# Kernel optimization log

Hardware: AMD Instinct MI355X
Metric: run time of the kernel (lower is better)

Reference implementation:

```python
import jax, jax.numpy as jnp
import numpy as np

D_MODEL = 768
D_LAT = 384
N_FREQ = D_MODEL // 2 + 1  # 385
INIT_S = 0.02


def _quat_linear(x, Ww, Wx, Wy, Wz, b):
    # Ww..Wz: [out_q, in_q]; x: [..., 4*in_q]
    d = Ww.shape[1]
    xw, xx, xy, xz = x[..., :d], x[..., d:2*d], x[..., 2*d:3*d], x[..., 3*d:]
    lin = lambda W, v: jnp.einsum('...i,oi->...o', v, W)
    ow = lin(Ww, xw) - lin(Wx, xx) - lin(Wy, xy) - lin(Wz, xz)
    ox = lin(Ww, xx) + lin(Wx, xw) + lin(Wy, xz) - lin(Wz, xy)
    oy = lin(Ww, xy) - lin(Wx, xz) + lin(Wy, xw) + lin(Wz, xx)
    oz = lin(Ww, xz) + lin(Wx, xy) - lin(Wy, xx) + lin(Wz, xw)
    return jnp.concatenate([ow, ox, oy, oz], axis=-1) + b


def _filter1d(x, kr, ki, n):
    X = jnp.fft.rfft(x, axis=-1)
    K = kr + 1j * ki
    return jnp.fft.irfft(X * K, n=n, axis=-1)


def setup_inputs() -> dict:
    key = jax.random.key(0)
    ks = jax.random.split(key, 16)
    rn = lambda k, shape: jax.random.normal(k, shape, dtype=jnp.float32)
    in_q_e, out_q_e = D_MODEL // 4, D_LAT // 4   # 192, 96
    in_q_d, out_q_d = D_LAT // 4, D_MODEL // 4   # 96, 192
    return {
        'x': rn(ks[0], (8, 4096, D_MODEL)),
        'enc_kr': rn(ks[1], (N_FREQ,)) * INIT_S,
        'enc_ki': rn(ks[2], (N_FREQ,)) * INIT_S,
        'dec_kr': rn(ks[3], (N_FREQ,)) * INIT_S,
        'dec_ki': rn(ks[4], (N_FREQ,)) * INIT_S,
        'enc_Ww': rn(ks[5], (out_q_e, in_q_e)) * 0.02,
        'enc_Wx': rn(ks[6], (out_q_e, in_q_e)) * 0.02,
        'enc_Wy': rn(ks[7], (out_q_e, in_q_e)) * 0.02,
        'enc_Wz': rn(ks[8], (out_q_e, in_q_e)) * 0.02,
        'enc_b': jnp.zeros((D_LAT,), jnp.float32),
        'dec_Ww': rn(ks[9], (out_q_d, in_q_d)) * 0.02,
        'dec_Wx': rn(ks[10], (out_q_d, in_q_d)) * 0.02,
        'dec_Wy': rn(ks[11], (out_q_d, in_q_d)) * 0.02,
        'dec_Wz': rn(ks[12], (out_q_d, in_q_d)) * 0.02,
        'dec_b': jnp.zeros((D_MODEL,), jnp.float32),
    }


def reference(x, enc_kr, enc_ki, dec_kr, dec_ki,
              enc_Ww, enc_Wx, enc_Wy, enc_Wz, enc_b,
              dec_Ww, dec_Wx, dec_Wy, dec_Wz, dec_b):
    # encode: spectral filter -> GELU (exact erf, matching nn.GELU) -> quaternion proj
    h = jax.nn.gelu(_filter1d(x, enc_kr, enc_ki, D_MODEL), approximate=False)
    z = _quat_linear(h, enc_Ww, enc_Wx, enc_Wy, enc_Wz, enc_b)
    # decode: quaternion proj -> spectral filter
    recon = _filter1d(_quat_linear(z, dec_Ww, dec_Wx, dec_Wy, dec_Wz, dec_b),
                      dec_kr, dec_ki, D_MODEL)
    loss = jnp.mean((recon - jax.lax.stop_gradient(x)) ** 2)
    return z, loss
```

## Files before the change

kernel.cpp:

```cpp
#include <hip/hip_runtime.h>
#include <hip/hip_bf16.h>
#include <math.h>

typedef unsigned short u16;
typedef __attribute__((ext_vector_type(8))) short s8v;
typedef __attribute__((ext_vector_type(4))) float f4v;

#define DM 768
#define DL 384

__device__ __forceinline__ u16 f2bf(float f) {
  union { float f; unsigned u; } v; v.f = f;
  unsigned r = v.u + 0x7fffu + ((v.u >> 16) & 1u);
  return (u16)(r >> 16);
}
__device__ __forceinline__ float bf2f(u16 b) {
  union { unsigned u; float f; } v; v.u = ((unsigned)b) << 16; return v.f;
}

__global__ void k_build_c2(const float* __restrict__ kr0, const float* __restrict__ ki0,
                           const float* __restrict__ kr1, const float* __restrict__ ki1,
                           float* __restrict__ c0, float* __restrict__ c1) {
  const float* kr = blockIdx.y ? kr1 : kr0;
  const float* ki = blockIdx.y ? ki1 : ki0;
  float* c = blockIdx.y ? c1 : c0;
  const int t = blockIdx.x;
  const int f = threadIdx.x;
  float s = 0.f;
  for (int ff = f; ff < 384; ff += 256) {
    if (ff >= 1) {
      int ph = (ff * t) % DM;
      float th = (float)ph * (6.283185307179586f / DM);
      float sn, cs; sincosf(th, &sn, &cs);
      s += 2.f * (kr[ff] * cs - ki[ff] * sn);
    }
  }
  if (f == 0) s += kr[0] + ((t & 1) ? -kr[384] : kr[384]);
  __shared__ float red[256];
  red[f] = s; __syncthreads();
  for (int k = 128; k > 0; k >>= 1) {
    if (f < k) red[f] += red[f + k];
    __syncthreads();
  }
  if (f == 0) c[t] = red[0] * (1.f / DM);
}

__global__ void k_rb2(const float* __restrict__ c, const float* __restrict__ b,
                      float* __restrict__ rb) {
  const int i = blockIdx.x;
  const int f = threadIdx.x;
  float s = 0.f;
  for (int j = f; j < DM; j += 256) {
    int ci = i - j; if (ci < 0) ci += DM;
    s += c[ci] * b[j];
  }
  __shared__ float red[256];
  red[f] = s; __syncthreads();
  for (int k = 128; k > 0; k >>= 1) {
    if (f < k) red[f] += red[f + k];
    __syncthreads();
  }
  if (f == 0) rb[i] = red[0];
}

__global__ void k_circ2(const float* __restrict__ c0, u16* __restrict__ B0,
                        const float* __restrict__ c1, u16* __restrict__ B1) {
  const float* c = blockIdx.y ? c1 : c0;
  u16* B = blockIdx.y ? B1 : B0;
  int idx = blockIdx.x * 256 + threadIdx.x;
  int i = idx / DM, j = idx % DM;
  int d = i - j; if (d < 0) d += DM;
  B[idx] = f2bf(c[d]);
}

__device__ __constant__ int   MI_[4][4] = {{0,1,2,3},{1,0,3,2},{2,3,0,1},{3,2,1,0}};
__device__ __constant__ float SG_[4][4] = {{1,-1,-1,-1},{1,1,-1,1},{1,1,1,-1},{1,-1,1,1}};

__global__ void k_wenc(const float* __restrict__ Ww, const float* __restrict__ Wx,
                       const float* __restrict__ Wy, const float* __restrict__ Wz,
                       u16* __restrict__ B) {
  int idx = blockIdx.x * 256 + threadIdx.x;
  int o = idx / DM, j = idx % DM;
  int p = o / 96, r = o % 96, q = j / 192, cc = j % 192;
  const float* Ws[4] = {Ww, Wx, Wy, Wz};
  B[idx] = f2bf(SG_[p][q] * Ws[MI_[p][q]][r * 192 + cc]);
}

__global__ void k_ddecT(const float* __restrict__ Ww, const float* __restrict__ Wx,
                        const float* __restrict__ Wy, const float* __restrict__ Wz,
                        u16* __restrict__ B) {
  int idx = blockIdx.x * 256 + threadIdx.x;
  int o = idx / DM, j = idx % DM;
  int p = j / 192, r = j % 192, q = o / 96, cc = o % 96;
  const float* Ws[4] = {Ww, Wx, Wy, Wz};
  B[idx] = f2bf(SG_[p][q] * Ws[MI_[p][q]][r * 96 + cc]);
}

__global__ void k_cvt(const float4* __restrict__ x, u16* __restrict__ xb) {
  int i = blockIdx.x * 256 + threadIdx.x;
  float4 v = x[i];
  union { u16 u[4]; unsigned long long q; } o;
  o.u[0] = f2bf(v.x); o.u[1] = f2bf(v.y); o.u[2] = f2bf(v.z); o.u[3] = f2bf(v.w);
  *(unsigned long long*)(xb + (size_t)i * 4) = o.q;
}

__device__ __forceinline__ void ld_lds16(const u16* g, u16* l) {
  __builtin_amdgcn_global_load_lds((const __attribute__((address_space(1))) void*)g,
                                   (__attribute__((address_space(3))) void*)l, 16, 0, 0);
}

__global__ __launch_bounds__(512, 1) void gemm8_g1(
    const u16* __restrict__ A, const u16* __restrict__ B, u16* __restrict__ outb) {
  __shared__ __align__(16) u16 SM[57344];
  const int t = threadIdx.x;
  const int lane = t & 63, wid = t >> 6;
  const int wrow = wid >> 2, wcol = wid & 3;
  int wg = blockIdx.x;
  { const int q = gridDim.x >> 3; wg = (wg & 7) * q + (wg >> 3); }
  const int bm = wg >> 2, bn = wg & 3;
  constexpr int KT = 768, NT = 768, NKT = KT / 64;

  f4v acc[8][3];
#pragma unroll
  for (int m = 0; m < 8; ++m)
#pragma unroll
    for (int n = 0; n < 3; ++n) acc[m][n] = (f4v)0.f;

  const int srow = t >> 3;
  const int sgrp = (t & 7) ^ (srow & 7);
  const u16* gA = A + (size_t)(bm * 256 + srow) * KT + sgrp * 8;
  const u16* gB = B + (size_t)(bn * 192 + srow) * KT + sgrp * 8;
  const int sx = ((lane >> 4) ^ (lane & 7)) * 8;
  const int ar = (wrow * 128 + (lane & 15)) * 64;
  const int br = 32768 + (wcol * 48 + (lane & 15)) * 64;

  auto stgA = [&](int kt_, int half_) {
    const u16* g = gA + (size_t)(half_ * 128) * KT + kt_ * 64;
    u16* l = SM + (kt_ & 1) * 16384 + half_ * 8192 + t * 8;
    ld_lds16(g, l);
    ld_lds16(g + 64 * KT, l + 4096);
  };
  auto stgB = [&](int kt_, int c_) {
    const u16* g = gB + (size_t)(c_ * 64) * KT + kt_ * 64;
    ld_lds16(g, SM + 32768 + (kt_ & 1) * 12288 + c_ * 4096 + t * 8);
  };

  stgA(0, 0); stgA(0, 1); stgB(0, 0); stgB(0, 1); stgB(0, 2);
  stgA(1, 0); stgB(1, 0);
  asm volatile("s_waitcnt vmcnt(3)" ::: "memory");
  __builtin_amdgcn_sched_barrier(0);
  __builtin_amdgcn_s_barrier();

#pragma unroll 2
  for (int kt = 0; kt < NKT; ++kt) {
    const int ca = (kt & 1) * 16384;
    const int cbb = (kt & 1) * 12288;
    s8v a0[4][2], a1[4][2], b01[2][2], b2[2];
#pragma unroll
    for (int m = 0; m < 4; ++m) {
      a0[m][0] = *(const s8v*)(SM + ca + ar + m * 1024 + sx);
      a0[m][1] = *(const s8v*)(SM + ca + ar + m * 1024 + (sx ^ 32));
    }
#pragma unroll
    for (int n = 0; n < 2; ++n) {
      b01[n][0] = *(const s8v*)(SM + cbb + br + n * 1024 + sx);
      b01[n][1] = *(const s8v*)(SM + cbb + br + n * 1024 + (sx ^ 32));
    }
    if (kt + 1 < NKT) stgA(kt + 1, 1);
    __builtin_amdgcn_s_barrier();
    asm volatile("s_waitcnt lgkmcnt(0)" ::: "memory");
    __builtin_amdgcn_sched_barrier(0);
    __builtin_amdgcn_s_setprio(1);
#pragma unroll
    for (int m = 0; m < 4; ++m)
#pragma unroll
      for (int n = 0; n < 2; ++n) {
        acc[m][n] = __builtin_amdgcn_mfma_f32_16x16x32_bf16(a0[m][0], b01[n][0], acc[m][n], 0, 0, 0);
        acc[m][n] = __builtin_amdgcn_mfma_f32_16x16x32_bf16(a0[m][1], b01[n][1], acc[m][n], 0, 0, 0);
      }
    __builtin_amdgcn_s_setprio(0);
    __builtin_amdgcn_s_barrier();
#pragma unroll
    for (int m = 0; m < 4; ++m) {
      a1[m][0] = *(const s8v*)(SM + ca + ar + (4 + m) * 1024 + sx);
      a1[m][1] = *(const s8v*)(SM + ca + ar + (4 + m) * 1024 + (sx ^ 32));
    }
    if (kt + 1 < NKT) { stgB(kt + 1, 1); stgB(kt + 1, 2); }
    __builtin_amdgcn_s_barrier();
    asm volatile("s_waitcnt lgkmcnt(0)" ::: "memory");
    __builtin_amdgcn_sched_barrier(0);
    __builtin_amdgcn_s_setprio(1);
#pragma unroll
    for (int m = 0; m < 4; ++m)
#pragma unroll
      for (int n = 0; n < 2; ++n) {
        acc[4 + m][n] = __builtin_amdgcn_mfma_f32_16x16x32_bf16(a1[m][0], b01[n][0], acc[4 + m][n], 0, 0, 0);
        acc[4 + m][n] = __builtin_amdgcn_mfma_f32_16x16x32_bf16(a1[m][1], b01[n][1], acc[4 + m][n], 0, 0, 0);
      }
    __builtin_amdgcn_s_setprio(0);
    __builtin_amdgcn_s_barrier();
    b2[0] = *(const s8v*)(SM + cbb + br + 2048 + sx);
    b2[1] = *(const s8v*)(SM + cbb + br + 2048 + (sx ^ 32));
    if (kt + 2 < NKT) stgA(kt + 2, 0);
    __builtin_amdgcn_s_barrier();
    asm volatile("s_waitcnt lgkmcnt(0)" ::: "memory");
    __builtin_amdgcn_sched_barrier(0);
    __builtin_amdgcn_s_setprio(1);
#pragma unroll
    for (int m = 0; m < 4; ++m) {
      acc[4 + m][2] = __builtin_amdgcn_mfma_f32_16x16x32_bf16(a1[m][0], b2[0], acc[4 + m][2], 0, 0, 0);
      acc[4 + m][2] = __builtin_amdgcn_mfma_f32_16x16x32_bf16(a1[m][1], b2[1], acc[4 + m][2], 0, 0, 0);
    }
    __builtin_amdgcn_s_setprio(0);
    __builtin_amdgcn_s_barrier();
    if (kt + 2 < NKT) {
      stgB(kt + 2, 0);
      asm volatile("s_waitcnt vmcnt(3)" ::: "memory");
    } else {
      asm volatile("s_waitcnt vmcnt(0)" ::: "memory");
    }
    __builtin_amdgcn_sched_barrier(0);
    __builtin_amdgcn_s_barrier();
    __builtin_amdgcn_s_setprio(1);
#pragma unroll
    for (int m = 0; m < 4; ++m) {
      acc[m][2] = __builtin_amdgcn_mfma_f32_16x16x32_bf16(a0[m][0], b2[0], acc[m][2], 0, 0, 0);
      acc[m][2] = __builtin_amdgcn_mfma_f32_16x16x32_bf16(a0[m][1], b2[1], acc[m][2], 0, 0, 0);
    }
    __builtin_amdgcn_s_setprio(0);
    __builtin_amdgcn_s_barrier();
  }

  for (int ch = 0; ch < 2; ++ch) {
    if (wrow == ch) {
#pragma unroll
      for (int m = 0; m < 8; ++m)
#pragma unroll
        for (int n = 0; n < 3; ++n)
#pragma unroll
          for (int j = 0; j < 4; ++j) {
            float v = acc[m][n][j];
            float u = v * 0.70710678118f, u2 = u * u;
            float p = u * (1.1283791671f + u2 * (-0.37612638903f +
                      u2 * (0.11283791671f + u2 * (-0.02686617064f))));
            v = 0.5f * v * (1.f + p);
            SM[(m * 16 + (lane >> 4) * 4 + j) * 200 + wcol * 48 + n * 16 + (lane & 15)] = f2bf(v);
          }
    }
    __syncthreads();
#pragma unroll
    for (int it = 0; it < 6; ++it) {
      int idx = it * 512 + t;
      int r = idx / 24, c8 = (idx % 24) * 8;
      s8v vv = *(const s8v*)(SM + r * 200 + c8);
      *(s8v*)(outb + (size_t)(bm * 256 + ch * 128 + r) * NT + bn * 192 + c8) = vv;
    }
    __syncthreads();
  }
}

template <int KT, int NT, int NBN, int EPI, int SWZ>
__global__ __launch_bounds__(256, 3) void gemm_ring(
    const u16* __restrict__ A, const u16* __restrict__ B,
    u16* __restrict__ outb, float* __restrict__ outf,
    const float* __restrict__ bias, const u16* __restrict__ xref,
    float* __restrict__ partials) {
  __shared__ __align__(16) u16 SMR[24576];
#define As_(b) (SMR + (b) * 4096)
#define Bs_(b) (SMR + 12288 + (b) * 4096)
  const int t = threadIdx.x;
  const int wid = t >> 6, lane = t & 63;
  const int wr = wid >> 1, wc = wid & 1;
  int wg = blockIdx.x;
  if (SWZ) { const int q = gridDim.x >> 3; wg = (wg & 7) * q + (wg >> 3); }
  const int bm = wg / NBN, bn = wg % NBN;

  f4v acc[4][4];
#pragma unroll
  for (int m = 0; m < 4; ++m)
#pragma unroll
    for (int n = 0; n < 4; ++n) acc[m][n] = (f4v)0.f;

  const int sgo = ((t & 3) ^ ((t >> 3) & 3)) * 8;
  const u16* gA = A + (size_t)(bm * 128 + (t >> 2)) * KT + sgo;
  const u16* gB = B + (size_t)(bn * 128 + (t >> 2)) * KT + sgo;
  const int fr = lane & 15;
  const int fo = ((lane >> 4) ^ ((fr >> 1) & 3)) * 8;
  constexpr int NK = KT / 32;

  auto stage = [&](int kt_, int b_) {
    const int ko = kt_ * 32;
    ld_lds16(gA + ko, As_(b_) + wid * 512);
    ld_lds16(gA + ko + 64 * KT, As_(b_) + wid * 512 + 2048);
    ld_lds16(gB + ko, Bs_(b_) + wid * 512);
    ld_lds16(gB + ko + 64 * KT, Bs_(b_) + wid * 512 + 2048);
  };

  stage(0, 0);
  stage(1, 1);
#pragma unroll 3
  for (int kt = 0; kt < NK; ++kt) {
    const int b0 = kt % 3, b2 = (kt + 2) % 3;
    if (kt + 2 < NK) stage(kt + 2, b2);
    const int ahead = NK - 1 - kt;
    if (ahead >= 2)      { asm volatile("s_waitcnt vmcnt(8)" ::: "memory"); }
    else if (ahead == 1) { asm volatile("s_waitcnt vmcnt(4)" ::: "memory"); }
    else                 { asm volatile("s_waitcnt vmcnt(0)" ::: "memory"); }
    __builtin_amdgcn_sched_barrier(0);
    __builtin_amdgcn_s_barrier();
    s8v af[4], bfv[4];
#pragma unroll
    for (int m = 0; m < 4; ++m)
      af[m] = *(const s8v*)(As_(b0) + (wr * 64 + m * 16 + fr) * 32 + fo);
#pragma unroll
    for (int n = 0; n < 4; ++n)
      bfv[n] = *(const s8v*)(Bs_(b0) + (wc * 64 + n * 16 + fr) * 32 + fo);
    asm volatile("s_waitcnt lgkmcnt(0)" ::: "memory");
    __builtin_amdgcn_sched_barrier(0);
    __builtin_amdgcn_s_barrier();
    __builtin_amdgcn_s_setprio(1);
#pragma unroll
    for (int m = 0; m < 4; ++m)
#pragma unroll
      for (int n = 0; n < 4; ++n)
        acc[m][n] = __builtin_amdgcn_mfma_f32_16x16x32_bf16(af[m], bfv[n], acc[m][n], 0, 0, 0);
    __builtin_amdgcn_s_setprio(0);
  }

  const int r0l = wr * 64 + ((lane >> 4) << 2);
  const int c0l = wc * 64 + (lane & 15);

  if constexpr (EPI == 2) {
    float bc[4];
#pragma unroll
    for (int n = 0; n < 4; ++n) bc[n] = bias[bn * 128 + c0l + n * 16];
    float ls = 0.f;
#pragma unroll
    for (int m = 0; m < 4; ++m)
#pragma unroll
      for (int n = 0; n < 4; ++n)
#pragma unroll
        for (int j = 0; j < 4; ++j) {
          size_t row = bm * 128 + r0l + m * 16 + j;
          int col = bn * 128 + c0l + n * 16;
          float v = acc[m][n][j] + bc[n];
          float d = v - bf2f(xref[row * NT + col]);
          ls += d * d;
        }
#pragma unroll
    for (int o = 32; o > 0; o >>= 1) ls += __shfl_down(ls, o);
    float* rw = (float*)SMR;
    if (lane == 0) rw[wid] = ls;
    __syncthreads();
    if (t == 0) partials[blockIdx.x] = rw[0] + rw[1] + rw[2] + rw[3];
  } else {
    u16* Cs = SMR;
    float bc[4];
    if constexpr (EPI == 1) {
#pragma unroll
      for (int n = 0; n < 4; ++n) bc[n] = bias[bn * 128 + c0l + n * 16];
    }
#pragma unroll
    for (int m = 0; m < 4; ++m)
#pragma unroll
      for (int n = 0; n < 4; ++n)
#pragma unroll
        for (int j = 0; j < 4; ++j) {
          float v = acc[m][n][j];
          if constexpr (EPI == 1) {
            v += bc[n];
            outf[(size_t)(bm * 128 + r0l + m * 16 + j) * NT + bn * 128 + c0l + n * 16] = v;
          }
          Cs[(r0l + m * 16 + j) * 130 + c0l + n * 16] = f2bf(v);
        }
    __syncthreads();
#pragma unroll
    for (int s = 0; s < 8; ++s) {
      int idx = (s * 256 + t) * 8;
      int r = idx >> 7, c = idx & 127;
      s8v vv = *(const s8v*)(Cs + r * 130 + c);
      *(s8v*)(outb + (size_t)(bm * 128 + r) * NT + bn * 128 + c) = vv;
    }
  }
#undef As_
#undef Bs_
}

__global__ void k_loss_final(const float* __restrict__ partials, float* __restrict__ out) {
  __shared__ float red[256];
  float s = 0.f;
  for (int i = threadIdx.x; i < 1536; i += 256) s += partials[i];
  red[threadIdx.x] = s; __syncthreads();
  for (int k = 128; k > 0; k >>= 1) {
    if (threadIdx.x < k) red[threadIdx.x] += red[threadIdx.x + k];
    __syncthreads();
  }
  if (threadIdx.x == 0) out[0] = red[0] / 25165824.f;
}

extern "C" void kernel_launch(void* const* d_in, const int* in_sizes, int n_in,
                              void* d_out, int out_size, void* d_ws, size_t ws_size,
                              hipStream_t stream) {
  const float* x      = (const float*)d_in[0];
  const float* enc_kr = (const float*)d_in[1];
  const float* enc_ki = (const float*)d_in[2];
  const float* dec_kr = (const float*)d_in[3];
  const float* dec_ki = (const float*)d_in[4];
  const float* enc_Ww = (const float*)d_in[5];
  const float* enc_Wx = (const float*)d_in[6];
  const float* enc_Wy = (const float*)d_in[7];
  const float* enc_Wz = (const float*)d_in[8];
  const float* enc_b  = (const float*)d_in[9];
  const float* dec_Ww = (const float*)d_in[10];
  const float* dec_Wx = (const float*)d_in[11];
  const float* dec_Wy = (const float*)d_in[12];
  const float* dec_Wz = (const float*)d_in[13];
  const float* dec_b  = (const float*)d_in[14];

  char* ws = (char*)d_ws;
  float* c_enc    = (float*)(ws + 0);
  float* c_dec    = (float*)(ws + 4096);
  float* rb       = (float*)(ws + 8192);
  float* partials = (float*)(ws + 12288);
  u16*   Benc     = (u16*)(ws + 20480);
  u16*   Wenc     = (u16*)(ws + 1200128);
  u16*   Mdec     = (u16*)(ws + 1789952);
  u16*   Cdec     = (u16*)(ws + 2379776);
  u16*   DdT      = (u16*)(ws + 3559424);
  u16*   Xb       = (u16*)(ws + 4149248);
  u16*   H        = (u16*)(ws + 54480896);
  u16*   Zb       = (u16*)(ws + 104812544);

  k_build_c2<<<dim3(768, 2), 256, 0, stream>>>(enc_kr, enc_ki, dec_kr, dec_ki, c_enc, c_dec);
  k_rb2<<<768, 256, 0, stream>>>(c_dec, dec_b, rb);
  k_circ2<<<dim3(2304, 2), 256, 0, stream>>>(c_enc, Benc, c_dec, Cdec);
  k_wenc<<<1152, 256, 0, stream>>>(enc_Ww, enc_Wx, enc_Wy, enc_Wz, Wenc);
  k_ddecT<<<1152, 256, 0, stream>>>(dec_Ww, dec_Wx, dec_Wy, dec_Wz, DdT);
  gemm_ring<768, 384, 3, 3, 0><<<18, 256, 0, stream>>>(Cdec, DdT, Mdec, nullptr, nullptr, nullptr, nullptr);
  k_cvt<<<24576, 256, 0, stream>>>((const float4*)x, Xb);

  float* zout = (float*)d_out;
  gemm8_g1<<<512, 512, 0, stream>>>(Xb, Benc, H);
  gemm_ring<768, 384, 3, 1, 1><<<768, 256, 0, stream>>>(H, Wenc, Zb, zout, enc_b, nullptr, nullptr);
  gemm_ring<384, 768, 6, 2, 1><<<1536, 256, 0, stream>>>(Zb, Mdec, nullptr, nullptr, rb, Xb, partials);
  k_loss_final<<<1, 256, 0, stream>>>(partials, zout + (out_size - 1));
}
```

Baseline: 167.1 us.

## Fuse encoder projection and decoder loss GEMMs into one kernel keeping Z in LDS

Replaces the two separate gemm_ring launches (H·Wenc producing Zb in global memory, then Zb·Mdec with loss epilogue) with one kernel. Each block computes a 128x384 Z tile, writes the fp32 z output, and stores a bf16 copy in swizzled LDS. It then runs the decoder GEMM from LDS in two 384-column chunks and accumulates the squared-error loss. This removes the Zb global round-trip and one launch. In exchange the grid drops to 256 blocks at one block per CU, and Mdec fragments are read straight from global memory with no LDS staging or prefetch, which may expose load latency.

```diff
diff --git a/kernel.cpp b/kernel.cpp
--- a/kernel.cpp
+++ b/kernel.cpp
@@ -259,21 +259,154 @@
   }
 }
 
-template <int KT, int NT, int NBN, int EPI, int SWZ>
+__global__ __launch_bounds__(512, 1) void gemm_zl(
+    const u16* __restrict__ H, const u16* __restrict__ Wenc,
+    const u16* __restrict__ Mdec, const u16* __restrict__ Xb,
+    const float* __restrict__ bias, const float* __restrict__ rb,
+    float* __restrict__ zout, float* __restrict__ partials) {
+  __shared__ __align__(16) u16 SM[49152];
+  const int t = threadIdx.x;
+  const int lane = t & 63, wid = t >> 6;
+  const int wrow = wid >> 2, wcol = wid & 3;
+  int wg = blockIdx.x;
+  { const int q = gridDim.x >> 3; wg = (wg & 7) * q + (wg >> 3); }
+  const int bm = wg;
+
+  f4v acc[4][6];
+#pragma unroll
+  for (int m = 0; m < 4; ++m)
+#pragma unroll
+    for (int n = 0; n < 6; ++n) acc[m][n] = (f4v)0.f;
+
+  const int sgo = ((t & 3) ^ ((t >> 3) & 3)) * 8;
+  const u16* gH = H + (size_t)(bm * 128 + (t >> 2)) * 768 + sgo;
+  const u16* gW = Wenc + (size_t)(t >> 2) * 768 + sgo;
+  const int fr = lane & 15;
+  const int fx = ((lane >> 4) ^ ((fr >> 1) & 3)) * 8;
+  const int arow = wrow * 64 + fr;
+
+  auto stage = [&](int kt_, int b_) {
+    ld_lds16(gH + kt_ * 32, SM + b_ * 4096 + t * 8);
+#pragma unroll
+    for (int i = 0; i < 3; ++i)
+      ld_lds16(gW + (size_t)i * 98304 + kt_ * 32, SM + 12288 + b_ * 12288 + i * 4096 + t * 8);
+  };
+
+  stage(0, 0);
+  stage(1, 1);
+#pragma unroll 3
+  for (int kt = 0; kt < 24; ++kt) {
+    const int b0 = kt % 3, b2 = (kt + 2) % 3;
+    if (kt + 2 < 24) stage(kt + 2, b2);
+    const int ahead = 23 - kt;
+    if (ahead >= 2)      { asm volatile("s_waitcnt vmcnt(8)" ::: "memory"); }
+    else if (ahead == 1) { asm volatile("s_waitcnt vmcnt(4)" ::: "memory"); }
+    else                 { asm volatile("s_waitcnt vmcnt(0)" ::: "memory"); }
+    __builtin_amdgcn_sched_barrier(0);
+    __builtin_amdgcn_s_barrier();
+    s8v af[4], bfv[6];
+#pragma unroll
+    for (int m = 0; m < 4; ++m)
+      af[m] = *(const s8v*)(SM + b0 * 4096 + (arow + m * 16) * 32 + fx);
+#pragma unroll
+    for (int n = 0; n < 6; ++n)
+      bfv[n] = *(const s8v*)(SM + 12288 + b0 * 12288 + (wcol * 96 + n * 16 + fr) * 32 + fx);
+    asm volatile("s_waitcnt lgkmcnt(0)" ::: "memory");
+    __builtin_amdgcn_sched_barrier(0);
+    __builtin_amdgcn_s_barrier();
+    __builtin_amdgcn_s_setprio(1);
+#pragma unroll
+    for (int m = 0; m < 4; ++m)
+#pragma unroll
+      for (int n = 0; n < 6; ++n)
+        acc[m][n] = __builtin_amdgcn_mfma_f32_16x16x32_bf16(af[m], bfv[n], acc[m][n], 0, 0, 0);
+    __builtin_amdgcn_s_setprio(0);
+  }
+  __syncthreads();
+
+  float bc[6];
+#pragma unroll
+  for (int n = 0; n < 6; ++n) bc[n] = bias[wcol * 96 + n * 16 + fr];
+#pragma unroll
+  for (int m = 0; m < 4; ++m)
+#pragma unroll
+    for (int n = 0; n < 6; ++n)
+#pragma unroll
+      for (int j = 0; j < 4; ++j) {
+        int rloc = wrow * 64 + m * 16 + (lane >> 4) * 4 + j;
+        int cloc = wcol * 96 + n * 16 + fr;
+        float v = acc[m][n][j] + bc[n];
+        zout[(size_t)(bm * 128 + rloc) * 384 + cloc] = v;
+        int g = cloc >> 3;
+        SM[rloc * 384 + ((g ^ (rloc & 7)) << 3) + (cloc & 7)] = f2bf(v);
+      }
+  __syncthreads();
+
+  float ls = 0.f;
+#pragma unroll 1
+  for (int chunk = 0; chunk < 2; ++chunk) {
+#pragma unroll
+    for (int m = 0; m < 4; ++m)
+#pragma unroll
+      for (int n = 0; n < 6; ++n) acc[m][n] = (f4v)0.f;
+#pragma unroll 3
+    for (int ks = 0; ks < 12; ++ks) {
+      s8v a2[4], b2[6];
+#pragma unroll
+      for (int m = 0; m < 4; ++m) {
+        int r = arow + m * 16;
+        a2[m] = *(const s8v*)(SM + r * 384 + (((ks * 4 + (lane >> 4)) ^ (fr & 7)) << 3));
+      }
+#pragma unroll
+      for (int n = 0; n < 6; ++n) {
+        int cR = chunk * 384 + wcol * 96 + n * 16 + fr;
+        b2[n] = *(const s8v*)(Mdec + (size_t)cR * 384 + ks * 32 + (lane >> 4) * 8);
+      }
+#pragma unroll
+      for (int m = 0; m < 4; ++m)
+#pragma unroll
+        for (int n = 0; n < 6; ++n)
+          acc[m][n] = __builtin_amdgcn_mfma_f32_16x16x32_bf16(a2[m], b2[n], acc[m][n], 0, 0, 0);
+    }
+#pragma unroll
+    for (int m = 0; m < 4; ++m)
+#pragma unroll
+      for (int n = 0; n < 6; ++n) {
+        int cg = chunk * 384 + wcol * 96 + n * 16 + fr;
+        float rbn = rb[cg];
+#pragma unroll
+        for (int j = 0; j < 4; ++j) {
+          int rg = bm * 128 + wrow * 64 + m * 16 + (lane >> 4) * 4 + j;
+          float rec = acc[m][n][j] + rbn;
+          float d = rec - bf2f(Xb[(size_t)rg * 768 + cg]);
+          ls += d * d;
+        }
+      }
+  }
+#pragma unroll
+  for (int o = 32; o > 0; o >>= 1) ls += __shfl_down(ls, o);
+  __syncthreads();
+  float* rw = (float*)SM;
+  if (lane == 0) rw[wid] = ls;
+  __syncthreads();
+  if (t == 0) {
+    float s = 0.f;
+#pragma unroll
+    for (int i = 0; i < 8; ++i) s += rw[i];
+    partials[blockIdx.x] = s;
+  }
+}
+
+template <int KT, int NT, int NBN>
 __global__ __launch_bounds__(256, 3) void gemm_ring(
-    const u16* __restrict__ A, const u16* __restrict__ B,
-    u16* __restrict__ outb, float* __restrict__ outf,
-    const float* __restrict__ bias, const u16* __restrict__ xref,
-    float* __restrict__ partials) {
+    const u16* __restrict__ A, const u16* __restrict__ B, u16* __restrict__ outb) {
   __shared__ __align__(16) u16 SMR[24576];
 #define As_(b) (SMR + (b) * 4096)
 #define Bs_(b) (SMR + 12288 + (b) * 4096)
   const int t = threadIdx.x;
   const int wid = t >> 6, lane = t & 63;
   const int wr = wid >> 1, wc = wid & 1;
-  int wg = blockIdx.x;
-  if (SWZ) { const int q = gridDim.x >> 3; wg = (wg & 7) * q + (wg >> 3); }
-  const int bm = wg / NBN, bn = wg % NBN;
+  const int bm = blockIdx.x / NBN, bn = blockIdx.x % NBN;
 
   f4v acc[4][4];
 #pragma unroll
@@ -329,58 +462,21 @@
 
   const int r0l = wr * 64 + ((lane >> 4) << 2);
   const int c0l = wc * 64 + (lane & 15);
-
-  if constexpr (EPI == 2) {
-    float bc[4];
-#pragma unroll
-    for (int n = 0; n < 4; ++n) bc[n] = bias[bn * 128 + c0l + n * 16];
-    float ls = 0.f;
-#pragma unroll
-    for (int m = 0; m < 4; ++m)
-#pragma unroll
-      for (int n = 0; n < 4; ++n)
-#pragma unroll
-        for (int j = 0; j < 4; ++j) {
-          size_t row = bm * 128 + r0l + m * 16 + j;
-          int col = bn * 128 + c0l + n * 16;
-          float v = acc[m][n][j] + bc[n];
-          float d = v - bf2f(xref[row * NT + col]);
-          ls += d * d;
-        }
-#pragma unroll
-    for (int o = 32; o > 0; o >>= 1) ls += __shfl_down(ls, o);
-    float* rw = (float*)SMR;
-    if (lane == 0) rw[wid] = ls;
-    __syncthreads();
-    if (t == 0) partials[blockIdx.x] = rw[0] + rw[1] + rw[2] + rw[3];
-  } else {
-    u16* Cs = SMR;
-    float bc[4];
-    if constexpr (EPI == 1) {
-#pragma unroll
-      for (int n = 0; n < 4; ++n) bc[n] = bias[bn * 128 + c0l + n * 16];
-    }
-#pragma unroll
-    for (int m = 0; m < 4; ++m)
-#pragma unroll
-      for (int n = 0; n < 4; ++n)
-#pragma unroll
-        for (int j = 0; j < 4; ++j) {
-          float v = acc[m][n][j];
-          if constexpr (EPI == 1) {
-            v += bc[n];
-            outf[(size_t)(bm * 128 + r0l + m * 16 + j) * NT + bn * 128 + c0l + n * 16] = v;
-          }
-          Cs[(r0l + m * 16 + j) * 130 + c0l + n * 16] = f2bf(v);
-        }
-    __syncthreads();
-#pragma unroll
-    for (int s = 0; s < 8; ++s) {
-      int idx = (s * 256 + t) * 8;
-      int r = idx >> 7, c = idx & 127;
-      s8v vv = *(const s8v*)(Cs + r * 130 + c);
-      *(s8v*)(outb + (size_t)(bm * 128 + r) * NT + bn * 128 + c) = vv;
-    }
+  u16* Cs = SMR;
+#pragma unroll
+  for (int m = 0; m < 4; ++m)
+#pragma unroll
+    for (int n = 0; n < 4; ++n)
+#pragma unroll
+      for (int j = 0; j < 4; ++j)
+        Cs[(r0l + m * 16 + j) * 130 + c0l + n * 16] = f2bf(acc[m][n][j]);
+  __syncthreads();
+#pragma unroll
+  for (int s = 0; s < 8; ++s) {
+    int idx = (s * 256 + t) * 8;
+    int r = idx >> 7, c = idx & 127;
+    s8v vv = *(const s8v*)(Cs + r * 130 + c);
+    *(s8v*)(outb + (size_t)(bm * 128 + r) * NT + bn * 128 + c) = vv;
   }
 #undef As_
 #undef Bs_
@@ -388,8 +484,7 @@
 
 __global__ void k_loss_final(const float* __restrict__ partials, float* __restrict__ out) {
   __shared__ float red[256];
-  float s = 0.f;
-  for (int i = threadIdx.x; i < 1536; i += 256) s += partials[i];
+  float s = partials[threadIdx.x];
   red[threadIdx.x] = s; __syncthreads();
   for (int k = 128; k > 0; k >>= 1) {
     if (threadIdx.x < k) red[threadIdx.x] += red[threadIdx.x + k];
@@ -429,19 +524,17 @@
   u16*   DdT      = (u16*)(ws + 3559424);
   u16*   Xb       = (u16*)(ws + 4149248);
   u16*   H        = (u16*)(ws + 54480896);
-  u16*   Zb       = (u16*)(ws + 104812544);
 
   k_build_c2<<<dim3(768, 2), 256, 0, stream>>>(enc_kr, enc_ki, dec_kr, dec_ki, c_enc, c_dec);
   k_rb2<<<768, 256, 0, stream>>>(c_dec, dec_b, rb);
   k_circ2<<<dim3(2304, 2), 256, 0, stream>>>(c_enc, Benc, c_dec, Cdec);
   k_wenc<<<1152, 256, 0, stream>>>(enc_Ww, enc_Wx, enc_Wy, enc_Wz, Wenc);
   k_ddecT<<<1152, 256, 0, stream>>>(dec_Ww, dec_Wx, dec_Wy, dec_Wz, DdT);
-  gemm_ring<768, 384, 3, 3, 0><<<18, 256, 0, stream>>>(Cdec, DdT, Mdec, nullptr, nullptr, nullptr, nullptr);
+  gemm_ring<768, 384, 3><<<18, 256, 0, stream>>>(Cdec, DdT, Mdec);
   k_cvt<<<24576, 256, 0, stream>>>((const float4*)x, Xb);
 
   float* zout = (float*)d_out;
   gemm8_g1<<<512, 512, 0, stream>>>(Xb, Benc, H);
-  gemm_ring<768, 384, 3, 1, 1><<<768, 256, 0, stream>>>(H, Wenc, Zb, zout, enc_b, nullptr, nullptr);
-  gemm_ring<384, 768, 6, 2, 1><<<1536, 256, 0, stream>>>(Zb, Mdec, nullptr, nullptr, rb, Xb, partials);
+  gemm_zl<<<256, 512, 0, stream>>>(H, Wenc, Mdec, Xb, enc_b, rb, zout, partials);
   k_loss_final<<<1, 256, 0, stream>>>(partials, zout + (out_size - 1));
 }
```

New measurement: 166.8 us. About the same (-0.1%).

## Fuse fp32-to-bf16 input conversion into first GEMM's A-tile staging

Applied to the files above, without the earlier changes.

Removes the separate k_cvt pass that converted x to bf16. The first GEMM now loads fp32 x into registers, converts it to bf16 and writes it to LDS inside its pipelined main loop. The loss epilogue reads fp32 x directly. This saves a full read and write of the 100MB input. In exchange the A tiles lose the async global-to-LDS loads and pay register pressure and conversion ALU inside the GEMM, and the A prefetch distance drops from two k-steps to one.

```diff
diff --git a/kernel.cpp b/kernel.cpp
--- a/kernel.cpp
+++ b/kernel.cpp
@@ -14,8 +14,8 @@
   unsigned r = v.u + 0x7fffu + ((v.u >> 16) & 1u);
   return (u16)(r >> 16);
 }
-__device__ __forceinline__ float bf2f(u16 b) {
-  union { unsigned u; float f; } v; v.u = ((unsigned)b) << 16; return v.f;
+__device__ __forceinline__ u16 f2bf_rne(float f) {
+  return __bfloat16_as_ushort(__float2bfloat16(f));
 }
 
 __global__ void k_build_c2(const float* __restrict__ kr0, const float* __restrict__ ki0,
@@ -96,21 +96,13 @@
   B[idx] = f2bf(SG_[p][q] * Ws[MI_[p][q]][r * 96 + cc]);
 }
 
-__global__ void k_cvt(const float4* __restrict__ x, u16* __restrict__ xb) {
-  int i = blockIdx.x * 256 + threadIdx.x;
-  float4 v = x[i];
-  union { u16 u[4]; unsigned long long q; } o;
-  o.u[0] = f2bf(v.x); o.u[1] = f2bf(v.y); o.u[2] = f2bf(v.z); o.u[3] = f2bf(v.w);
-  *(unsigned long long*)(xb + (size_t)i * 4) = o.q;
-}
-
 __device__ __forceinline__ void ld_lds16(const u16* g, u16* l) {
   __builtin_amdgcn_global_load_lds((const __attribute__((address_space(1))) void*)g,
                                    (__attribute__((address_space(3))) void*)l, 16, 0, 0);
 }
 
-__global__ __launch_bounds__(512, 1) void gemm8_g1(
-    const u16* __restrict__ A, const u16* __restrict__ B, u16* __restrict__ outb) {
+__global__ __launch_bounds__(512, 1) void gemm8f_g1(
+    const float* __restrict__ X, const u16* __restrict__ B, u16* __restrict__ outb) {
   __shared__ __align__(16) u16 SM[57344];
   const int t = threadIdx.x;
   const int lane = t & 63, wid = t >> 6;
@@ -128,26 +120,48 @@
 
   const int srow = t >> 3;
   const int sgrp = (t & 7) ^ (srow & 7);
-  const u16* gA = A + (size_t)(bm * 256 + srow) * KT + sgrp * 8;
-  const u16* gB = B + (size_t)(bn * 192 + srow) * KT + sgrp * 8;
+  const float* gX = X + (size_t)(bm * 256 + srow) * KT + sgrp * 8;
+  const u16*   gB = B + (size_t)(bn * 192 + srow) * KT + sgrp * 8;
   const int sx = ((lane >> 4) ^ (lane & 7)) * 8;
   const int ar = (wrow * 128 + (lane & 15)) * 64;
   const int br = 32768 + (wcol * 48 + (lane & 15)) * 64;
 
-  auto stgA = [&](int kt_, int half_) {
-    const u16* g = gA + (size_t)(half_ * 128) * KT + kt_ * 64;
-    u16* l = SM + (kt_ & 1) * 16384 + half_ * 8192 + t * 8;
-    ld_lds16(g, l);
-    ld_lds16(g + 64 * KT, l + 4096);
-  };
   auto stgB = [&](int kt_, int c_) {
     const u16* g = gB + (size_t)(c_ * 64) * KT + kt_ * 64;
     ld_lds16(g, SM + 32768 + (kt_ & 1) * 12288 + c_ * 4096 + t * 8);
   };
-
-  stgA(0, 0); stgA(0, 1); stgB(0, 0); stgB(0, 1); stgB(0, 2);
-  stgA(1, 0); stgB(1, 0);
-  asm volatile("s_waitcnt vmcnt(3)" ::: "memory");
+  float4 ra0[4], ra1[4];
+  auto LA = [&](int kt_, int half_, float4* r) {
+    const float* g = gX + (size_t)(half_ * 128) * KT + kt_ * 64;
+    r[0] = *(const float4*)(g);
+    r[1] = *(const float4*)(g + 4);
+    r[2] = *(const float4*)(g + 64 * KT);
+    r[3] = *(const float4*)(g + 64 * KT + 4);
+  };
+  auto WA = [&](int kt_, int half_, const float4* r) {
+    union { u16 u[8]; s8v s; } w0, w1;
+    w0.u[0] = f2bf_rne(r[0].x); w0.u[1] = f2bf_rne(r[0].y);
+    w0.u[2] = f2bf_rne(r[0].z); w0.u[3] = f2bf_rne(r[0].w);
+    w0.u[4] = f2bf_rne(r[1].x); w0.u[5] = f2bf_rne(r[1].y);
+    w0.u[6] = f2bf_rne(r[1].z); w0.u[7] = f2bf_rne(r[1].w);
+    w1.u[0] = f2bf_rne(r[2].x); w1.u[1] = f2bf_rne(r[2].y);
+    w1.u[2] = f2bf_rne(r[2].z); w1.u[3] = f2bf_rne(r[2].w);
+    w1.u[4] = f2bf_rne(r[3].x); w1.u[5] = f2bf_rne(r[3].y);
+    w1.u[6] = f2bf_rne(r[3].z); w1.u[7] = f2bf_rne(r[3].w);
+    u16* l = SM + (kt_ & 1) * 16384 + half_ * 8192 + t * 8;
+    *(s8v*)l = w0.s;
+    *(s8v*)(l + 4096) = w1.s;
+  };
+
+  stgB(0, 0); stgB(0, 1); stgB(0, 2);
+  LA(0, 0, ra0); LA(0, 1, ra1);
+  asm volatile("s_waitcnt vmcnt(4)" ::: "memory");
+  __builtin_amdgcn_sched_barrier(0);
+  WA(0, 0, ra0);
+  asm volatile("s_waitcnt vmcnt(0)" ::: "memory");
+  __builtin_amdgcn_sched_barrier(0);
+  WA(0, 1, ra1);
+  asm volatile("s_waitcnt lgkmcnt(0)" ::: "memory");
   __builtin_amdgcn_sched_barrier(0);
   __builtin_amdgcn_s_barrier();
 
@@ -166,7 +180,10 @@
       b01[n][0] = *(const s8v*)(SM + cbb + br + n * 1024 + sx);
       b01[n][1] = *(const s8v*)(SM + cbb + br + n * 1024 + (sx ^ 32));
     }
-    if (kt + 1 < NKT) stgA(kt + 1, 1);
+    if (kt + 1 < NKT) {
+      stgB(kt + 1, 0); stgB(kt + 1, 1); stgB(kt + 1, 2);
+      LA(kt + 1, 0, ra0);
+    }
     __builtin_amdgcn_s_barrier();
     asm volatile("s_waitcnt lgkmcnt(0)" ::: "memory");
     __builtin_amdgcn_sched_barrier(0);
@@ -185,7 +202,7 @@
       a1[m][0] = *(const s8v*)(SM + ca + ar + (4 + m) * 1024 + sx);
       a1[m][1] = *(const s8v*)(SM + ca + ar + (4 + m) * 1024 + (sx ^ 32));
     }
-    if (kt + 1 < NKT) { stgB(kt + 1, 1); stgB(kt + 1, 2); }
+    if (kt + 1 < NKT) LA(kt + 1, 1, ra1);
     __builtin_amdgcn_s_barrier();
     asm volatile("s_waitcnt lgkmcnt(0)" ::: "memory");
     __builtin_amdgcn_sched_barrier(0);
@@ -201,7 +218,11 @@
     __builtin_amdgcn_s_barrier();
     b2[0] = *(const s8v*)(SM + cbb + br + 2048 + sx);
     b2[1] = *(const s8v*)(SM + cbb + br + 2048 + (sx ^ 32));
-    if (kt + 2 < NKT) stgA(kt + 2, 0);
+    if (kt + 1 < NKT) {
+      asm volatile("s_waitcnt vmcnt(4)" ::: "memory");
+      __builtin_amdgcn_sched_barrier(0);
+      WA(kt + 1, 0, ra0);
+    }
     __builtin_amdgcn_s_barrier();
     asm volatile("s_waitcnt lgkmcnt(0)" ::: "memory");
     __builtin_amdgcn_sched_barrier(0);
@@ -213,14 +234,14 @@
     }
     __builtin_amdgcn_s_setprio(0);
     __builtin_amdgcn_s_barrier();
-    if (kt + 2 < NKT) {
-      stgB(kt + 2, 0);
-      asm volatile("s_waitcnt vmcnt(3)" ::: "memory");
-    } else {
+    if (kt + 1 < NKT) {
       asm volatile("s_waitcnt vmcnt(0)" ::: "memory");
-    }
-    __builtin_amdgcn_sched_barrier(0);
-    __builtin_amdgcn_s_barrier();
+      __builtin_amdgcn_sched_barrier(0);
+      WA(kt + 1, 1, ra1);
+    }
+    __builtin_amdgcn_s_barrier();
+    asm volatile("s_waitcnt lgkmcnt(0)" ::: "memory");
+    __builtin_amdgcn_sched_barrier(0);
     __builtin_amdgcn_s_setprio(1);
 #pragma unroll
     for (int m = 0; m < 4; ++m) {
@@ -263,7 +284,7 @@
 __global__ __launch_bounds__(256, 3) void gemm_ring(
     const u16* __restrict__ A, const u16* __restrict__ B,
     u16* __restrict__ outb, float* __restrict__ outf,
-    const float* __restrict__ bias, const u16* __restrict__ xref,
+    const float* __restrict__ bias, const float* __restrict__ xref,
     float* __restrict__ partials) {
   __shared__ __align__(16) u16 SMR[24576];
 #define As_(b) (SMR + (b) * 4096)
@@ -344,7 +365,7 @@
           size_t row = bm * 128 + r0l + m * 16 + j;
           int col = bn * 128 + c0l + n * 16;
           float v = acc[m][n][j] + bc[n];
-          float d = v - bf2f(xref[row * NT + col]);
+          float d = v - xref[row * NT + col];
           ls += d * d;
         }
 #pragma unroll
@@ -427,9 +448,8 @@
   u16*   Mdec     = (u16*)(ws + 1789952);
   u16*   Cdec     = (u16*)(ws + 2379776);
   u16*   DdT      = (u16*)(ws + 3559424);
-  u16*   Xb       = (u16*)(ws + 4149248);
-  u16*   H        = (u16*)(ws + 54480896);
-  u16*   Zb       = (u16*)(ws + 104812544);
+  u16*   Zb       = (u16*)(ws + 4149248);
+  u16*   H        = (u16*)(ws + 29315072);
 
   k_build_c2<<<dim3(768, 2), 256, 0, stream>>>(enc_kr, enc_ki, dec_kr, dec_ki, c_enc, c_dec);
   k_rb2<<<768, 256, 0, stream>>>(c_dec, dec_b, rb);
@@ -437,11 +457,10 @@
   k_wenc<<<1152, 256, 0, stream>>>(enc_Ww, enc_Wx, enc_Wy, enc_Wz, Wenc);
   k_ddecT<<<1152, 256, 0, stream>>>(dec_Ww, dec_Wx, dec_Wy, dec_Wz, DdT);
   gemm_ring<768, 384, 3, 3, 0><<<18, 256, 0, stream>>>(Cdec, DdT, Mdec, nullptr, nullptr, nullptr, nullptr);
-  k_cvt<<<24576, 256, 0, stream>>>((const float4*)x, Xb);
 
   float* zout = (float*)d_out;
-  gemm8_g1<<<512, 512, 0, stream>>>(Xb, Benc, H);
+  gemm8f_g1<<<512, 512, 0, stream>>>(x, Benc, H);
   gemm_ring<768, 384, 3, 1, 1><<<768, 256, 0, stream>>>(H, Wenc, Zb, zout, enc_b, nullptr, nullptr);
-  gemm_ring<384, 768, 6, 2, 1><<<1536, 256, 0, stream>>>(Zb, Mdec, nullptr, nullptr, rb, Xb, partials);
+  gemm_ring<384, 768, 6, 2, 1><<<1536, 256, 0, stream>>>(Zb, Mdec, nullptr, nullptr, rb, x, partials);
   k_loss_final<<<1, 256, 0, stream>>>(partials, zout + (out_size - 1));
 }
```

Result: faster. 153.5 us (median of 3 runs) (-8.1%).
